# Kernel tuning notes

Hardware: AMD Instinct MI355X
Metric: run time of the kernel (lower is better)

## Reference

```python
import jax, jax.numpy as jnp
import numpy as np

B, S, D = 32, 256, 768
H = 12
HD = D // H           # 64
MLP = 4 * D           # 3072
EPS = 1e-5


def layernorm(x, g, b):
    mu = jnp.mean(x, axis=-1, keepdims=True)
    var = jnp.mean((x - mu) ** 2, axis=-1, keepdims=True)
    return (x - mu) * jax.lax.rsqrt(var + EPS) * g + b


def setup_inputs() -> dict:
    key = jax.random.key(0)
    ks = jax.random.split(key, 16)
    s_head = 1.0 / np.sqrt(HD)
    s_d = 1.0 / np.sqrt(D)
    s_mlp = 1.0 / np.sqrt(MLP)
    return {
        "x": jax.random.normal(ks[0], (B, S, D), dtype=jnp.float32),
        "g1": jnp.ones((D,), jnp.float32),
        "beta1": jnp.zeros((D,), jnp.float32),
        # per-head linear weights, torch Linear layout [out, in] stacked over heads
        "Wq": jax.random.uniform(ks[1], (H, HD, HD), jnp.float32, -s_head, s_head),
        "bq": jax.random.uniform(ks[2], (H, HD), jnp.float32, -s_head, s_head),
        "Wk": jax.random.uniform(ks[3], (H, HD, HD), jnp.float32, -s_head, s_head),
        "bk": jax.random.uniform(ks[4], (H, HD), jnp.float32, -s_head, s_head),
        "Wv": jax.random.uniform(ks[5], (H, HD, HD), jnp.float32, -s_head, s_head),
        "bv": jax.random.uniform(ks[6], (H, HD), jnp.float32, -s_head, s_head),
        "g2": jnp.ones((D,), jnp.float32),
        "beta2": jnp.zeros((D,), jnp.float32),
        "W1": jax.random.uniform(ks[7], (MLP, D), jnp.float32, -s_d, s_d),
        "bm1": jax.random.uniform(ks[8], (MLP,), jnp.float32, -s_d, s_d),
        "W2": jax.random.uniform(ks[9], (D, MLP), jnp.float32, -s_mlp, s_mlp),
        "bm2": jax.random.uniform(ks[10], (D,), jnp.float32, -s_mlp, s_mlp),
    }


def reference(x, g1, beta1, Wq, bq, Wk, bk, Wv, bv, g2, beta2, W1, bm1, W2, bm2):
    # --- MHA on norm1(x), fused over batch and heads ---
    h = layernorm(x, g1, beta1)                      # [B,S,D]
    hh = h.reshape(B, S, H, HD)                      # head split matches slicing in Mymha
    # q_e = sum_d hh_d * W[e,d]  (torch Linear: y = x @ W.T + b)
    q = jnp.einsum('bshd,hed->bshe', hh, Wq) + bq
    k = jnp.einsum('bshd,hed->bshe', hh, Wk) + bk
    v = jnp.einsum('bshd,hed->bshe', hh, Wv) + bv
    scores = jnp.einsum('bshe,bthe->bhst', q, k) / np.sqrt(HD)
    attn = jax.nn.softmax(scores, axis=-1)           # [B,H,S,S]
    ctx = jnp.einsum('bhst,bthe->bshe', attn, v).reshape(B, S, D)
    out = ctx + x
    # --- MLP on norm2(out) ---
    h2 = layernorm(out, g2, beta2)
    m = jax.nn.gelu(h2 @ W1.T + bm1, approximate=False)  # torch nn.GELU is exact erf
    out = m @ W2.T + bm2 + out
    return out
```

## Files before the change

kernel.cpp:

```cpp
#include <hip/hip_runtime.h>
#include <hip/hip_bf16.h>
#include <math.h>


static constexpr int Bn = 32, Sn = 256, Dn = 768, Hn = 12, HDn = 64, MLPn = 3072;
static constexpr int NT = Bn * Sn;

typedef unsigned short ushort_t;
typedef unsigned int u32;
typedef __attribute__((ext_vector_type(8))) short short8;
typedef __attribute__((ext_vector_type(4))) float f32x4;

__device__ __forceinline__ float bf2f(ushort_t u) { return __uint_as_float(((u32)u) << 16); }
__device__ __forceinline__ ushort_t f2bf(float f) {
  u32 u = __float_as_uint(f);
  u += 0x7fffu + ((u >> 16) & 1u);
  return (ushort_t)(u >> 16);
}

__device__ __forceinline__ void async_cp16(const ushort_t* g, ushort_t* l) {
  __builtin_amdgcn_global_load_lds(
      (const __attribute__((address_space(1))) u32*)g,
      (__attribute__((address_space(3))) u32*)l, 16, 0, 0);
}

__global__ __launch_bounds__(256) void k_prep(
    const float* __restrict__ Wq, const float* __restrict__ Wk,
    const float* __restrict__ Wv, const float* __restrict__ bq,
    const float* __restrict__ bk, const float* __restrict__ bv,
    const float* __restrict__ W1, const float* __restrict__ W2,
    const float* __restrict__ x, const float* __restrict__ g1,
    const float* __restrict__ be1,
    ushort_t* __restrict__ Wc, float* __restrict__ bc,
    ushort_t* __restrict__ W1b, ushort_t* __restrict__ W2b,
    ushort_t* __restrict__ hb)
{
  __shared__ float red[8];
  const int bx = blockIdx.x;
  const int tid = threadIdx.x;
  if (bx < 576) {
    int i = bx * 256 + tid;
    int h = i / 12288, rem = i - h * 12288;
    int mat = rem / 4096, w = rem - mat * 4096;
    const float* src = (mat == 0) ? Wq : ((mat == 1) ? Wk : Wv);
    Wc[i] = f2bf(src[h * 4096 + w]);
    if (i < Hn * 192) {
      int h2 = i / 192, r2 = i - h2 * 192;
      int m2 = r2 / 64, e2 = r2 - m2 * 64;
      const float* bs = (m2 == 0) ? bq : ((m2 == 1) ? bk : bv);
      bc[i] = bs[h2 * 64 + e2];
    }
  } else if (bx < 5184) {
    int j = bx - 576;
    const float* src = (j < 2304) ? W1 : W2;
    ushort_t* dst = (j < 2304) ? W1b : W2b;
    int i = (j % 2304) * 256 + tid;
    float4 v = ((const float4*)src)[i];
    ushort4 o;
    o.x = f2bf(v.x); o.y = f2bf(v.y); o.z = f2bf(v.z); o.w = f2bf(v.w);
    ((ushort4*)dst)[i] = o;
  } else {
    const int t = bx - 5184;
    float xv[3];
#pragma unroll
    for (int i = 0; i < 3; i++) xv[i] = x[(size_t)t * Dn + tid + i * 256];
    float s = xv[0] + xv[1] + xv[2];
#pragma unroll
    for (int off = 32; off > 0; off >>= 1) s += __shfl_down(s, off, 64);
    if ((tid & 63) == 0) red[tid >> 6] = s;
    __syncthreads();
    float mean = (red[0] + red[1] + red[2] + red[3]) * (1.0f / 768.0f);
    float d0 = xv[0] - mean, d1 = xv[1] - mean, d2 = xv[2] - mean;
    float s2 = d0 * d0 + d1 * d1 + d2 * d2;
#pragma unroll
    for (int off = 32; off > 0; off >>= 1) s2 += __shfl_down(s2, off, 64);
    if ((tid & 63) == 0) red[4 + (tid >> 6)] = s2;
    __syncthreads();
    float rstd = rsqrtf((red[4] + red[5] + red[6] + red[7]) * (1.0f / 768.0f) + 1e-5f);
#pragma unroll
    for (int i = 0; i < 3; i++) {
      int d = tid + i * 256;
      hb[(size_t)t * Dn + d] = f2bf((xv[i] - mean) * rstd * g1[d] + be1[d]);
    }
  }
}

__global__ __launch_bounds__(256) void k_qkv(
    const ushort_t* __restrict__ hb,
    const ushort_t* __restrict__ Wc,
    const float* __restrict__ bc,
    ushort_t* __restrict__ qo, ushort_t* __restrict__ ko, ushort_t* __restrict__ vt)
{
  __shared__ __align__(16) ushort_t As[128 * 72];
  __shared__ __align__(16) ushort_t Ws[192 * 72];
  const int blk = blockIdx.x;
  const int half = blk & 1;
  const int bh = blk >> 1;
  const int b_ = bh / Hn, h_ = bh - b_ * Hn;
  const int tid = threadIdx.x;
  const int t0 = b_ * Sn + half * 128;

  {
    int row = tid >> 1, seg = (tid & 1) * 32;
    const uint4* g = (const uint4*)(hb + (size_t)(t0 + row) * Dn + h_ * 64 + seg);
    uint4* s = (uint4*)(As + row * 72 + seg);
    s[0] = g[0]; s[1] = g[1]; s[2] = g[2]; s[3] = g[3];
  }
  {
    int rr = tid >> 2, seg = (tid & 3) * 16;
    const ushort_t* gw = Wc + h_ * 12288;
#pragma unroll
    for (int p = 0; p < 3; p++) {
      int R = p * 64 + rr;
      const uint4* g = (const uint4*)(gw + R * 64 + seg);
      uint4* s = (uint4*)(Ws + R * 72 + seg);
      s[0] = g[0]; s[1] = g[1];
    }
  }
  __syncthreads();

  const int wave = tid >> 6, lane = tid & 63;
  const int wm = (wave >> 1) * 64, wn = (wave & 1) * 96;
  const int lrow = lane & 15, quad = lane >> 4;

  f32x4 acc[4][6];
#pragma unroll
  for (int mi = 0; mi < 4; mi++)
#pragma unroll
    for (int ni = 0; ni < 6; ni++) acc[mi][ni] = (f32x4){0.f, 0.f, 0.f, 0.f};

#pragma unroll
  for (int kk = 0; kk < 2; kk++) {
    short8 af[4], wf[6];
#pragma unroll
    for (int mi = 0; mi < 4; mi++)
      af[mi] = *(const short8*)(As + (wm + mi * 16 + lrow) * 72 + kk * 32 + quad * 8);
#pragma unroll
    for (int ni = 0; ni < 6; ni++)
      wf[ni] = *(const short8*)(Ws + (wn + ni * 16 + lrow) * 72 + kk * 32 + quad * 8);
#pragma unroll
    for (int mi = 0; mi < 4; mi++)
#pragma unroll
      for (int ni = 0; ni < 6; ni++)
        acc[mi][ni] = __builtin_amdgcn_mfma_f32_16x16x32_bf16(af[mi], wf[ni], acc[mi][ni], 0, 0, 0);
  }

#pragma unroll
  for (int ni = 0; ni < 6; ni++) {
    int c = wn + ni * 16 + lrow;
    int mat = c >> 6, e = c & 63;
    float bb = bc[h_ * 192 + c];
    if (mat < 2) {
      ushort_t* dst = (mat == 0) ? qo : ko;
      size_t base = (((size_t)bh) * Sn + half * 128 + wm) * HDn + e;
#pragma unroll
      for (int mi = 0; mi < 4; mi++) {
#pragma unroll
        for (int r = 0; r < 4; r++) {
          int lr = mi * 16 + quad * 4 + r;
          dst[base + (size_t)lr * HDn] = f2bf(acc[mi][ni][r] + bb);
        }
      }
    } else {
      size_t rowb = ((size_t)bh * 64 + e) * Sn + half * 128 + wm + quad * 4;
#pragma unroll
      for (int mi = 0; mi < 4; mi++) {
        ushort4 pk;
        pk.x = f2bf(acc[mi][ni][0] + bb);
        pk.y = f2bf(acc[mi][ni][1] + bb);
        pk.z = f2bf(acc[mi][ni][2] + bb);
        pk.w = f2bf(acc[mi][ni][3] + bb);
        *(ushort4*)(vt + rowb + mi * 16) = pk;
      }
    }
  }
}

__global__ __launch_bounds__(256) void k_attn(
    const ushort_t* __restrict__ q,
    const ushort_t* __restrict__ kg_,
    const ushort_t* __restrict__ vt,
    const float* __restrict__ x,
    float* __restrict__ out1)
{
  __shared__ __align__(16) ushort_t Ks[64 * 72];
  __shared__ __align__(16) ushort_t Vts[64 * 264];
  __shared__ __align__(16) ushort_t Pw[4][16 * 72];
  const int blk = blockIdx.x;
  const int qtr = blk & 3, bh = blk >> 2;
  const int b_ = bh / Hn, h_ = bh - b_ * Hn;
  const int tid = threadIdx.x, wave = tid >> 6, lane = tid & 63;
  const int lr16 = lane & 15, quad = lane >> 4;
  const int s0 = qtr * 64 + wave * 16;

  {
    int r = tid >> 2, cseg = (tid & 3) * 64;
    const uint4* g = (const uint4*)(vt + ((size_t)bh * 64 + r) * Sn + cseg);
    uint4* s = (uint4*)(Vts + r * 264 + cseg);
#pragma unroll
    for (int i = 0; i < 8; i++) s[i] = g[i];
  }

  short8 qf[2];
  {
    const ushort_t* qg = q + ((size_t)bh * Sn + s0 + lr16) * HDn + quad * 8;
    qf[0] = *(const short8*)(qg);
    qf[1] = *(const short8*)(qg + 32);
  }

  f32x4 of[4];
#pragma unroll
  for (int et = 0; et < 4; et++) of[et] = (f32x4){0.f, 0.f, 0.f, 0.f};
  float mrow[4] = {-3.0e38f, -3.0e38f, -3.0e38f, -3.0e38f};
  float lsum[4] = {0.f, 0.f, 0.f, 0.f};

  const ushort_t* kgb = kg_ + (size_t)bh * Sn * HDn;

  for (int c = 0; c < 4; c++) {
    if (c) __syncthreads();
    {
      int row = tid >> 2, seg = (tid & 3) * 16;
      const uint4* g = (const uint4*)(kgb + (size_t)(c * 64 + row) * HDn + seg);
      uint4* s = (uint4*)(Ks + row * 72 + seg);
      s[0] = g[0]; s[1] = g[1];
    }
    __syncthreads();

    f32x4 sc[4];
#pragma unroll
    for (int ni = 0; ni < 4; ni++) sc[ni] = (f32x4){0.f, 0.f, 0.f, 0.f};
#pragma unroll
    for (int kk = 0; kk < 2; kk++) {
#pragma unroll
      for (int ni = 0; ni < 4; ni++) {
        short8 kf = *(const short8*)(Ks + (ni * 16 + lr16) * 72 + kk * 32 + quad * 8);
        sc[ni] = __builtin_amdgcn_mfma_f32_16x16x32_bf16(qf[kk], kf, sc[ni], 0, 0, 0);
      }
    }

    float alpha[4];
#pragma unroll
    for (int r = 0; r < 4; r++) {
      float m_ = fmaxf(fmaxf(sc[0][r], sc[1][r]), fmaxf(sc[2][r], sc[3][r]));
#pragma unroll
      for (int msk = 8; msk >= 1; msk >>= 1) m_ = fmaxf(m_, __shfl_xor(m_, msk, 64));
      float mn = fmaxf(mrow[r], m_);
      alpha[r] = __expf((mrow[r] - mn) * 0.125f);
      mrow[r] = mn;
    }
#pragma unroll
    for (int ni = 0; ni < 4; ni++) {
#pragma unroll
      for (int r = 0; r < 4; r++) {
        float p = __expf((sc[ni][r] - mrow[r]) * 0.125f);
        sc[ni][r] = p;
        Pw[wave][(quad * 4 + r) * 72 + ni * 16 + lr16] = f2bf(p);
      }
    }
#pragma unroll
    for (int r = 0; r < 4; r++) {
      float s_ = (sc[0][r] + sc[1][r]) + (sc[2][r] + sc[3][r]);
#pragma unroll
      for (int msk = 8; msk >= 1; msk >>= 1) s_ += __shfl_xor(s_, msk, 64);
      lsum[r] = lsum[r] * alpha[r] + s_;
    }
#pragma unroll
    for (int et = 0; et < 4; et++)
#pragma unroll
      for (int r = 0; r < 4; r++) of[et][r] *= alpha[r];

    short8 pf0 = *(const short8*)(&Pw[wave][lr16 * 72 + quad * 8]);
    short8 pf1 = *(const short8*)(&Pw[wave][lr16 * 72 + 32 + quad * 8]);
#pragma unroll
    for (int et = 0; et < 4; et++) {
      short8 vf0 = *(const short8*)(Vts + (et * 16 + lr16) * 264 + c * 64 + quad * 8);
      short8 vf1 = *(const short8*)(Vts + (et * 16 + lr16) * 264 + c * 64 + 32 + quad * 8);
      of[et] = __builtin_amdgcn_mfma_f32_16x16x32_bf16(pf0, vf0, of[et], 0, 0, 0);
      of[et] = __builtin_amdgcn_mfma_f32_16x16x32_bf16(pf1, vf1, of[et], 0, 0, 0);
    }
  }

  const size_t obase = ((size_t)b_ * Sn + s0) * Dn + h_ * 64;
#pragma unroll
  for (int r = 0; r < 4; r++) {
    float rl = 1.0f / lsum[r];
    int row = quad * 4 + r;
#pragma unroll
    for (int et = 0; et < 4; et++) {
      size_t idx = obase + (size_t)row * Dn + et * 16 + lr16;
      out1[idx] = of[et][r] * rl + x[idx];
    }
  }
}

__global__ __launch_bounds__(256) void k_ln2(
    const float* __restrict__ in, const float* __restrict__ g2,
    const float* __restrict__ be2, ushort_t* __restrict__ h2)
{
  const int t = blockIdx.x, tid = threadIdx.x;
  __shared__ float red[8];
  float xv[3];
#pragma unroll
  for (int i = 0; i < 3; i++) xv[i] = in[(size_t)t * Dn + tid + i * 256];
  float s = xv[0] + xv[1] + xv[2];
#pragma unroll
  for (int off = 32; off > 0; off >>= 1) s += __shfl_down(s, off, 64);
  if ((tid & 63) == 0) red[tid >> 6] = s;
  __syncthreads();
  float mean = (red[0] + red[1] + red[2] + red[3]) * (1.0f / 768.0f);
  float d0 = xv[0] - mean, d1 = xv[1] - mean, d2 = xv[2] - mean;
  float s2 = d0 * d0 + d1 * d1 + d2 * d2;
#pragma unroll
  for (int off = 32; off > 0; off >>= 1) s2 += __shfl_down(s2, off, 64);
  if ((tid & 63) == 0) red[4 + (tid >> 6)] = s2;
  __syncthreads();
  float rstd = rsqrtf((red[4] + red[5] + red[6] + red[7]) * (1.0f / 768.0f) + 1e-5f);
#pragma unroll
  for (int i = 0; i < 3; i++) {
    int d = tid + i * 256;
    h2[(size_t)t * Dn + d] = f2bf((xv[i] - mean) * rstd * g2[d] + be2[d]);
  }
}

__global__ __launch_bounds__(512) void k_gemm1(
    const ushort_t* __restrict__ A,
    const ushort_t* __restrict__ Bw,
    const float* __restrict__ bias,
    ushort_t* __restrict__ CoutB)
{
  constexpr int KDIM = Dn, N = MLPn;
  __shared__ __align__(16) ushort_t smem[24576];
  ushort_t* As0 = smem;
  ushort_t* Bs0 = smem + 8192;
  ushort_t* As1 = smem + 12288;
  ushort_t* Bs1 = smem + 20480;
  ushort_t* Cs = smem;
  const int b = blockIdx.x;
  const int xcd = b & 7, slot = b >> 3;
  const int cc = slot % 24, rloc = slot / 24;
  const int m0 = (xcd * 4 + rloc) * 256, n0 = cc * 128;
  const int tid = threadIdx.x;
  const int wave = tid >> 6, lane = tid & 63;
  const int wm = (wave >> 1) << 6, wn = (wave & 1) << 6;
  const int lrow = lane & 15, quad = lane >> 4;
  const int lrow4 = lane >> 2;
  const int lcol8s = (((lane & 3) ^ ((lane >> 3) & 3))) * 8;
  const int qsw = ((quad ^ ((lrow >> 1) & 3))) * 8;

  f32x4 acc[4][4];
#pragma unroll
  for (int mi = 0; mi < 4; mi++)
#pragma unroll
    for (int ni = 0; ni < 4; ni++) acc[mi][ni] = (f32x4){0.f, 0.f, 0.f, 0.f};

  auto stage = [&](int k0, ushort_t* Ad, ushort_t* Bd) {
    async_cp16(A + (size_t)(m0 + wave * 16 + lrow4) * KDIM + k0 + lcol8s,
               Ad + (wave * 16) * 32);
    async_cp16(A + (size_t)(m0 + 128 + wave * 16 + lrow4) * KDIM + k0 + lcol8s,
               Ad + (128 + wave * 16) * 32);
    async_cp16(Bw + (size_t)(n0 + wave * 16 + lrow4) * KDIM + k0 + lcol8s,
               Bd + (wave * 16) * 32);
  };
  auto compute = [&](const ushort_t* As_, const ushort_t* Bs_) {
    short8 af[4], bfv[4];
#pragma unroll
    for (int mi = 0; mi < 4; mi++)
      af[mi] = *(const short8*)(As_ + (wm + mi * 16 + lrow) * 32 + qsw);
#pragma unroll
    for (int ni = 0; ni < 4; ni++)
      bfv[ni] = *(const short8*)(Bs_ + (wn + ni * 16 + lrow) * 32 + qsw);
#pragma unroll
    for (int mi = 0; mi < 4; mi++)
#pragma unroll
      for (int ni = 0; ni < 4; ni++)
        acc[mi][ni] = __builtin_amdgcn_mfma_f32_16x16x32_bf16(af[mi], bfv[ni], acc[mi][ni], 0, 0, 0);
  };

  stage(0, As0, Bs0);
  __syncthreads();
  for (int k0 = 0; k0 < KDIM; k0 += 64) {
    stage(k0 + 32, As1, Bs1);
    compute(As0, Bs0);
    __syncthreads();
    if (k0 + 64 < KDIM) stage(k0 + 64, As0, Bs0);
    compute(As1, Bs1);
    __syncthreads();
  }

#pragma unroll
  for (int p = 0; p < 2; p++) {
    if ((wm >> 7) == p) {
#pragma unroll
      for (int ni = 0; ni < 4; ni++) {
        int col = wn + ni * 16 + lrow;
        float bc = bias[n0 + col];
#pragma unroll
        for (int mi = 0; mi < 4; mi++) {
#pragma unroll
          for (int r = 0; r < 4; r++) {
            float vv = acc[mi][ni][r] + bc;
            float u = vv * (0.7978845608f + 0.0356774081f * vv * vv);
            float o = vv / (1.0f + __expf(-2.0f * u));
            Cs[((wm & 127) + mi * 16 + quad * 4 + r) * 136 + col] = f2bf(o);
          }
        }
      }
    }
    __syncthreads();
    int row = tid >> 2, part = tid & 3;
    const uint4* s = (const uint4*)(Cs + row * 136 + part * 32);
    uint4* d = (uint4*)(CoutB + (size_t)(m0 + p * 128 + row) * N + n0 + part * 32);
#pragma unroll
    for (int i = 0; i < 4; i++) d[i] = s[i];
    if (p == 0) __syncthreads();
  }
}

__global__ __launch_bounds__(256) void k_gemm2(
    const ushort_t* __restrict__ A,
    const ushort_t* __restrict__ Bw,
    const float* __restrict__ bias,
    const float* __restrict__ res,
    float* __restrict__ out)
{
  constexpr int KDIM = MLPn, N = Dn;
  __shared__ __align__(16) ushort_t smem[24576];
  ushort_t* As0 = smem;
  ushort_t* Bs0 = smem + 4096;
  ushort_t* As1 = smem + 12288;
  ushort_t* Bs1 = smem + 16384;
  const int b = blockIdx.x;
  const int xcd = b & 7, slot = b >> 3;
  const int cc = slot % 6, rloc = slot / 6;
  const int m0 = (xcd * 16 + rloc) * 64, n0 = cc * 128;
  const int tid = threadIdx.x;
  const int wave = tid >> 6, lane = tid & 63;
  const int wm = (wave >> 1) << 5, wn = (wave & 1) << 6;
  const int lrow = lane & 15, quad = lane >> 4;
  const int r8 = lane >> 3;
  const int c8s = (((lane & 7) ^ ((lane >> 3) & 7))) * 8;
  const int qsw2[2] = { ((0 * 4 + quad) ^ (lrow & 7)) * 8,
                        ((1 * 4 + quad) ^ (lrow & 7)) * 8 };

  f32x4 acc[2][4];
#pragma unroll
  for (int mi = 0; mi < 2; mi++)
#pragma unroll
    for (int ni = 0; ni < 4; ni++) acc[mi][ni] = (f32x4){0.f, 0.f, 0.f, 0.f};

  auto stage = [&](int k0, ushort_t* Ad, ushort_t* Bd) {
    async_cp16(A + (size_t)(m0 + wave * 8 + r8) * KDIM + k0 + c8s,
               Ad + (wave * 8) * 64);
    async_cp16(A + (size_t)(m0 + 32 + wave * 8 + r8) * KDIM + k0 + c8s,
               Ad + (32 + wave * 8) * 64);
#pragma unroll
    for (int g = 0; g < 4; g++)
      async_cp16(Bw + (size_t)(n0 + g * 32 + wave * 8 + r8) * KDIM + k0 + c8s,
                 Bd + (g * 32 + wave * 8) * 64);
  };
  auto compute = [&](const ushort_t* As_, const ushort_t* Bs_) {
#pragma unroll
    for (int kk = 0; kk < 2; kk++) {
      short8 af[2], bfv[4];
#pragma unroll
      for (int mi = 0; mi < 2; mi++)
        af[mi] = *(const short8*)(As_ + (wm + mi * 16 + lrow) * 64 + qsw2[kk]);
#pragma unroll
      for (int ni = 0; ni < 4; ni++)
        bfv[ni] = *(const short8*)(Bs_ + (wn + ni * 16 + lrow) * 64 + qsw2[kk]);
#pragma unroll
      for (int mi = 0; mi < 2; mi++)
#pragma unroll
        for (int ni = 0; ni < 4; ni++)
          acc[mi][ni] = __builtin_amdgcn_mfma_f32_16x16x32_bf16(af[mi], bfv[ni], acc[mi][ni], 0, 0, 0);
    }
  };

  stage(0, As0, Bs0);
  __syncthreads();
  for (int k0 = 0; k0 < KDIM; k0 += 128) {
    stage(k0 + 64, As1, Bs1);
    compute(As0, Bs0);
    __syncthreads();
    if (k0 + 128 < KDIM) stage(k0 + 128, As0, Bs0);
    compute(As1, Bs1);
    __syncthreads();
  }

#pragma unroll
  for (int ni = 0; ni < 4; ni++) {
    int col = n0 + wn + ni * 16 + lrow;
    float bc = bias[col];
#pragma unroll
    for (int mi = 0; mi < 2; mi++) {
#pragma unroll
      for (int r = 0; r < 4; r++) {
        int row = m0 + wm + mi * 16 + quad * 4 + r;
        size_t idx = (size_t)row * N + col;
        out[idx] = acc[mi][ni][r] + bc + res[idx];
      }
    }
  }
}

extern "C" void kernel_launch(void* const* d_in, const int* in_sizes, int n_in,
                              void* d_out, int out_size, void* d_ws, size_t ws_size,
                              hipStream_t stream) {
  (void)in_sizes; (void)n_in; (void)out_size; (void)ws_size;
  const float* x   = (const float*)d_in[0];
  const float* g1  = (const float*)d_in[1];
  const float* be1 = (const float*)d_in[2];
  const float* Wq  = (const float*)d_in[3];
  const float* bq  = (const float*)d_in[4];
  const float* Wk  = (const float*)d_in[5];
  const float* bk  = (const float*)d_in[6];
  const float* Wv  = (const float*)d_in[7];
  const float* bv  = (const float*)d_in[8];
  const float* g2  = (const float*)d_in[9];
  const float* be2 = (const float*)d_in[10];
  const float* W1  = (const float*)d_in[11];
  const float* bm1 = (const float*)d_in[12];
  const float* W2  = (const float*)d_in[13];
  const float* bm2 = (const float*)d_in[14];
  float* outp = (float*)d_out;

  char* ws = (char*)d_ws;
  float*    out1 = (float*)ws;
  ushort_t* hb   = (ushort_t*)ws;
  ushort_t* qb   = (ushort_t*)(ws + 25165824);
  ushort_t* kb   = (ushort_t*)(ws + 37748736);
  ushort_t* vtb  = (ushort_t*)(ws + 50331648);
  ushort_t* h2   = qb;
  ushort_t* mb   = (ushort_t*)(ws + 37748736);
  ushort_t* Wc   = (ushort_t*)(ws + 88080384);
  ushort_t* W1b  = (ushort_t*)(ws + 88375296);
  ushort_t* W2b  = (ushort_t*)(ws + 93093888);
  float*    bcb  = (float*)(ws + 97812480);

  k_prep<<<dim3(5184 + NT), dim3(256), 0, stream>>>(Wq, Wk, Wv, bq, bk, bv, W1, W2,
                                                    x, g1, be1, Wc, bcb, W1b, W2b, hb);
  k_qkv<<<dim3(Bn * Hn * 2), dim3(256), 0, stream>>>(hb, Wc, bcb, qb, kb, vtb);
  k_attn<<<dim3(Bn * Hn * 4), dim3(256), 0, stream>>>(qb, kb, vtb, x, out1);
  k_ln2<<<dim3(NT), dim3(256), 0, stream>>>(out1, g2, be2, h2);
  k_gemm1<<<dim3(768), dim3(512), 0, stream>>>(h2, W1b, bm1, mb);
  k_gemm2<<<dim3(768), dim3(256), 0, stream>>>(mb, W2b, bm2, out1, outp);
}
```

Before: 286.2 us.

## Keep two async loads in flight with counted vmcnt waits in MLP GEMMs

Both MLP GEMM main loops are restructured so the next two K-stages are always in flight. Partial s_waitcnt vmcnt counts replace the full __syncthreads drains, and sched_barrier fences pin the instruction order. MFMA blocks are also wrapped in s_setprio to raise wave priority during compute. This aims to hide global-to-LDS latency behind MFMA work. The cost is fragile hand-counted wait values and hardcoded trip counts tied to KDIM.

```diff
diff --git a/kernel.cpp b/kernel.cpp
--- a/kernel.cpp
+++ b/kernel.cpp
@@ -369,23 +369,46 @@
 #pragma unroll
     for (int ni = 0; ni < 4; ni++)
       bfv[ni] = *(const short8*)(Bs_ + (wn + ni * 16 + lrow) * 32 + qsw);
+    __builtin_amdgcn_s_setprio(1);
 #pragma unroll
     for (int mi = 0; mi < 4; mi++)
 #pragma unroll
       for (int ni = 0; ni < 4; ni++)
         acc[mi][ni] = __builtin_amdgcn_mfma_f32_16x16x32_bf16(af[mi], bfv[ni], acc[mi][ni], 0, 0, 0);
+    __builtin_amdgcn_s_setprio(0);
   };
 
   stage(0, As0, Bs0);
+  stage(32, As1, Bs1);
+  for (int s = 0; s < 22; s += 2) {
+    __builtin_amdgcn_sched_barrier(0);
+    asm volatile("s_waitcnt vmcnt(3)" ::: "memory");
+    __builtin_amdgcn_s_barrier();
+    __builtin_amdgcn_sched_barrier(0);
+    compute(As0, Bs0);
+    __builtin_amdgcn_s_barrier();
+    __builtin_amdgcn_sched_barrier(0);
+    stage((s + 2) * 32, As0, Bs0);
+    __builtin_amdgcn_sched_barrier(0);
+    asm volatile("s_waitcnt vmcnt(3)" ::: "memory");
+    __builtin_amdgcn_s_barrier();
+    __builtin_amdgcn_sched_barrier(0);
+    compute(As1, Bs1);
+    __builtin_amdgcn_s_barrier();
+    __builtin_amdgcn_sched_barrier(0);
+    stage((s + 3) * 32, As1, Bs1);
+  }
+  __builtin_amdgcn_sched_barrier(0);
+  asm volatile("s_waitcnt vmcnt(3)" ::: "memory");
+  __builtin_amdgcn_s_barrier();
+  __builtin_amdgcn_sched_barrier(0);
+  compute(As0, Bs0);
+  __builtin_amdgcn_sched_barrier(0);
+  asm volatile("s_waitcnt vmcnt(0)" ::: "memory");
+  __builtin_amdgcn_s_barrier();
+  __builtin_amdgcn_sched_barrier(0);
+  compute(As1, Bs1);
   __syncthreads();
-  for (int k0 = 0; k0 < KDIM; k0 += 64) {
-    stage(k0 + 32, As1, Bs1);
-    compute(As0, Bs0);
-    __syncthreads();
-    if (k0 + 64 < KDIM) stage(k0 + 64, As0, Bs0);
-    compute(As1, Bs1);
-    __syncthreads();
-  }
 
 #pragma unroll
   for (int p = 0; p < 2; p++) {
@@ -468,24 +491,46 @@
 #pragma unroll
       for (int ni = 0; ni < 4; ni++)
         bfv[ni] = *(const short8*)(Bs_ + (wn + ni * 16 + lrow) * 64 + qsw2[kk]);
+      __builtin_amdgcn_s_setprio(1);
 #pragma unroll
       for (int mi = 0; mi < 2; mi++)
 #pragma unroll
         for (int ni = 0; ni < 4; ni++)
           acc[mi][ni] = __builtin_amdgcn_mfma_f32_16x16x32_bf16(af[mi], bfv[ni], acc[mi][ni], 0, 0, 0);
+      __builtin_amdgcn_s_setprio(0);
     }
   };
 
   stage(0, As0, Bs0);
-  __syncthreads();
-  for (int k0 = 0; k0 < KDIM; k0 += 128) {
-    stage(k0 + 64, As1, Bs1);
+  stage(64, As1, Bs1);
+  for (int s = 0; s < 46; s += 2) {
+    __builtin_amdgcn_sched_barrier(0);
+    asm volatile("s_waitcnt vmcnt(6)" ::: "memory");
+    __builtin_amdgcn_s_barrier();
+    __builtin_amdgcn_sched_barrier(0);
     compute(As0, Bs0);
-    __syncthreads();
-    if (k0 + 128 < KDIM) stage(k0 + 128, As0, Bs0);
+    __builtin_amdgcn_s_barrier();
+    __builtin_amdgcn_sched_barrier(0);
+    stage((s + 2) * 64, As0, Bs0);
+    __builtin_amdgcn_sched_barrier(0);
+    asm volatile("s_waitcnt vmcnt(6)" ::: "memory");
+    __builtin_amdgcn_s_barrier();
+    __builtin_amdgcn_sched_barrier(0);
     compute(As1, Bs1);
-    __syncthreads();
-  }
+    __builtin_amdgcn_s_barrier();
+    __builtin_amdgcn_sched_barrier(0);
+    stage((s + 3) * 64, As1, Bs1);
+  }
+  __builtin_amdgcn_sched_barrier(0);
+  asm volatile("s_waitcnt vmcnt(6)" ::: "memory");
+  __builtin_amdgcn_s_barrier();
+  __builtin_amdgcn_sched_barrier(0);
+  compute(As0, Bs0);
+  __builtin_amdgcn_sched_barrier(0);
+  asm volatile("s_waitcnt vmcnt(0)" ::: "memory");
+  __builtin_amdgcn_s_barrier();
+  __builtin_amdgcn_sched_barrier(0);
+  compute(As1, Bs1);
 
 #pragma unroll
   for (int ni = 0; ni < 4; ni++) {
```

Measured after the change: 292.9 us. 2.3% more time.
